# Optimization experiments

Hardware: AMD Instinct MI355X
Metric: run time of the kernel (lower is better)

Reference implementation:

```python
import jax, jax.numpy as jnp
import numpy as np

B, C, T, H, W = 8, 3, 16, 64, 64
CIN = C * T          # 48, conv in_channels
CQK = CIN // 8       # 6, query/key channels


def setup_inputs() -> dict:
    key = jax.random.key(0)
    ks = jax.random.split(key, 8)
    s = 0.05
    return {
        "x": jax.random.normal(ks[0], (B, C, T, H, W), dtype=jnp.float32),
        "Wq": jax.random.normal(ks[1], (CQK, CIN), dtype=jnp.float32) * s,
        "bq": jax.random.normal(ks[2], (CQK,), dtype=jnp.float32) * s,
        "Wk": jax.random.normal(ks[3], (CQK, CIN), dtype=jnp.float32) * s,
        "bk": jax.random.normal(ks[4], (CQK,), dtype=jnp.float32) * s,
        "Wv": jax.random.normal(ks[5], (CIN, CIN), dtype=jnp.float32) * s,
        "bv": jax.random.normal(ks[6], (CIN,), dtype=jnp.float32) * s,
        "gamma": jax.random.normal(ks[7], (1,), dtype=jnp.float32) * s,
    }


def reference(x, Wq, bq, Wk, bk, Wv, bv, gamma):
    b, c, t, h, w = x.shape
    n = h * w
    # merge channel and time dims: [B, C*T, H*W]
    x2 = x.reshape(b, c * t, n)
    # 1x1 convs are per-position channel matmuls
    q = jnp.einsum('oc,bcn->bon', Wq, x2) + bq[None, :, None]   # [B, CQK, N]
    k = jnp.einsum('oc,bcn->bon', Wk, x2) + bk[None, :, None]   # [B, CQK, N]
    v = jnp.einsum('oc,bcn->bon', Wv, x2) + bv[None, :, None]   # [B, CIN, N]
    # energy[b, i, j] = <q[:, i], k[:, j]>
    energy = jnp.einsum('bci,bcj->bij', q, k)                   # [B, N, N]
    attn = jax.nn.softmax(energy, axis=-1)
    # out[b, c, i] = sum_j v[b, c, j] * attn[b, i, j]
    out = jnp.einsum('bcj,bij->bci', v, attn)                   # [B, CIN, N]
    out = gamma[0] * out + x2
    return out.reshape(b, c, t, h, w)
```

## Files before the change

kernel.cpp:

```cpp
#include <hip/hip_runtime.h>

#define B_    8
#define CIN   48
#define CQK   6
#define N_    4096
#define CV    64
#define TI    64
#define TJ    64
#define NCH   4
#define JCH   (N_ / NCH)
#define TILES (JCH / TJ)

typedef __attribute__((ext_vector_type(8)))  short short8;
typedef __attribute__((ext_vector_type(16))) float f32x16;

__device__ __forceinline__ unsigned short f2bf(float f) {
    unsigned int u = __float_as_uint(f);
    u += 0x7FFFu + ((u >> 16) & 1u);
    return (unsigned short)(u >> 16);
}

__device__ __forceinline__ unsigned int cvt_pk_bf16(float a, float b) {
    unsigned int r;
    asm("v_cvt_pk_bf16_f32 %0, %1, %2" : "=v"(r) : "v"(a), "v"(b));
    return r;
}

__device__ __forceinline__ void pl32swap(unsigned int& x, unsigned int& y) {
    asm("v_permlane32_swap_b32 %0, %1" : "+v"(x), "+v"(y));
}

__device__ __forceinline__ short8 mk8(unsigned int w0, unsigned int w1,
                                      unsigned int w2, unsigned int w3) {
    union { unsigned int u[4]; short8 s; } t;
    t.u[0] = w0; t.u[1] = w1; t.u[2] = w2; t.u[3] = w3;
    return t.s;
}

__global__ __launch_bounds__(256) void qkv_kernel(
    const float* __restrict__ x,
    const float* __restrict__ Wq, const float* __restrict__ bq,
    const float* __restrict__ Wk, const float* __restrict__ bk,
    const float* __restrict__ Wv, const float* __restrict__ bv,
    unsigned short* __restrict__ qB, unsigned short* __restrict__ kB,
    unsigned short* __restrict__ vB)
{
    __shared__ float sWq[CQK * CIN], sWk[CQK * CIN], sWv[CIN * CIN];
    __shared__ float sbq[CQK], sbk[CQK], sbv[CIN];
    const int tid = threadIdx.x;
    for (int idx = tid; idx < CQK * CIN; idx += 256) { sWq[idx] = Wq[idx]; sWk[idx] = Wk[idx]; }
    for (int idx = tid; idx < CIN * CIN; idx += 256) sWv[idx] = Wv[idx];
    if (tid < CQK) { sbq[tid] = bq[tid]; sbk[tid] = bk[tid]; }
    if (tid < CIN) sbv[tid] = bv[tid];
    __syncthreads();

    const int b = blockIdx.x >> 6;
    const int g = tid >> 6;
    const int n = ((blockIdx.x & 63) << 6) + (tid & 63);

    float xc[CIN];
    const float* xb = x + ((size_t)b * CIN) * N_ + n;
#pragma unroll
    for (int c = 0; c < CIN; ++c) xc[c] = xb[(size_t)c * N_];

    if (g == 0) {
        short8 qrow = {0,0,0,0,0,0,0,0}, krow = {0,0,0,0,0,0,0,0};
#pragma unroll
        for (int o = 0; o < CQK; ++o) {
            float sq = sbq[o], sk = sbk[o];
#pragma unroll
            for (int c = 0; c < CIN; ++c) {
                sq += sWq[o * CIN + c] * xc[c];
                sk += sWk[o * CIN + c] * xc[c];
            }
            qrow[o] = (short)f2bf(sq);
            krow[o] = (short)f2bf(sk);
        }
        *(short8*)&qB[((size_t)b * N_ + n) * 8] = qrow;
        *(short8*)&kB[((size_t)b * N_ + n) * 8] = krow;
        vB[((size_t)b * CV + 48) * N_ + n] = 0x3F80u;
#pragma unroll
        for (int o = 49; o < CV; ++o) vB[((size_t)b * CV + o) * N_ + n] = 0;
    } else {
        const int o0 = (g - 1) * 16;
#pragma unroll
        for (int oo = 0; oo < 16; ++oo) {
            const int o = o0 + oo;
            float sv = sbv[o];
#pragma unroll
            for (int c = 0; c < CIN; ++c) sv += sWv[o * CIN + c] * xc[c];
            vB[((size_t)b * CV + o) * N_ + n] = f2bf(sv);
        }
    }
}

__global__ __launch_bounds__(512, 4) void attn_kernel(
    const unsigned short* __restrict__ qB, const unsigned short* __restrict__ kB,
    const unsigned short* __restrict__ vB, const float* __restrict__ x,
    const float* __restrict__ gamma, float* __restrict__ out)
{
    __shared__ unsigned short vt[NCH][CV][TJ];
    __shared__ float cbuf[CV][TI + 1];

    const int tid   = threadIdx.x;
    const int l     = tid & 63;
    const int w     = tid >> 6;
    const int chunk = w & 3;
    const int iw    = w >> 2;
    const int hi    = l >> 5;
    const int li    = l & 31;
    const int b     = blockIdx.x >> 6;
    const int ig    = blockIdx.x & 63;
    const int i_base = ig * TI;

    const unsigned short* kg = kB + (size_t)b * N_ * 8;
    const unsigned short* vg = vB + (size_t)b * CV * N_;

    short8 qf = {0,0,0,0,0,0,0,0};
    if (hi == 0)
        qf = *(const short8*)&qB[((size_t)b * N_ + i_base + iw * 32 + li) * 8];

    f32x16 zc, acc0, acc1;
#pragma unroll
    for (int r = 0; r < 16; ++r) { zc[r] = 0.f; acc0[r] = 0.f; acc1[r] = 0.f; }

#define DO_JST(JST, KF)                                                        \
    {                                                                          \
        f32x16 s = __builtin_amdgcn_mfma_f32_32x32x16_bf16(KF, qf, zc, 0, 0, 0);\
        _Pragma("unroll")                                                      \
        for (int r = 0; r < 16; ++r) s[r] = __expf(s[r]);                      \
        unsigned int c00 = cvt_pk_bf16(s[0],  s[1]);                           \
        unsigned int c10 = cvt_pk_bf16(s[2],  s[3]);                           \
        unsigned int c01 = cvt_pk_bf16(s[4],  s[5]);                           \
        unsigned int c11 = cvt_pk_bf16(s[6],  s[7]);                           \
        unsigned int c02 = cvt_pk_bf16(s[8],  s[9]);                           \
        unsigned int c12 = cvt_pk_bf16(s[10], s[11]);                          \
        unsigned int c03 = cvt_pk_bf16(s[12], s[13]);                          \
        unsigned int c13 = cvt_pk_bf16(s[14], s[15]);                          \
        unsigned int x0 = c00, y0 = c01; pl32swap(x0, y0);                     \
        unsigned int x1 = c10, y1 = c11; pl32swap(x1, y1);                     \
        const short8 pa0 = mk8(x0, x1, y0, y1);                                \
        unsigned int x2 = c02, y2 = c03; pl32swap(x2, y2);                     \
        unsigned int x3 = c12, y3 = c13; pl32swap(x3, y3);                     \
        const short8 pa1 = mk8(x2, x3, y2, y3);                                \
        const char* vrow0 = (const char*)&vt[chunk][li][0];                    \
        const char* vrow1 = (const char*)&vt[chunk][32 + li][0];               \
        short8 vf;                                                             \
        vf = *(const short8*)(vrow0 + ((((JST)*4 + 0 + hi) ^ (li & 7)) << 4)); \
        acc0 = __builtin_amdgcn_mfma_f32_32x32x16_bf16(pa0, vf, acc0, 0, 0, 0);\
        vf = *(const short8*)(vrow0 + ((((JST)*4 + 2 + hi) ^ (li & 7)) << 4)); \
        acc0 = __builtin_amdgcn_mfma_f32_32x32x16_bf16(pa1, vf, acc0, 0, 0, 0);\
        vf = *(const short8*)(vrow1 + ((((JST)*4 + 0 + hi) ^ (li & 7)) << 4)); \
        acc1 = __builtin_amdgcn_mfma_f32_32x32x16_bf16(pa0, vf, acc1, 0, 0, 0);\
        vf = *(const short8*)(vrow1 + ((((JST)*4 + 2 + hi) ^ (li & 7)) << 4)); \
        acc1 = __builtin_amdgcn_mfma_f32_32x32x16_bf16(pa1, vf, acc1, 0, 0, 0);\
    }

#pragma unroll 1
    for (int t = 0; t < TILES; ++t) {
        const int j0 = chunk * JCH + t * TJ;

        short8 kf0 = {0,0,0,0,0,0,0,0}, kf1 = {0,0,0,0,0,0,0,0};
        if (hi == 0) {
            kf0 = *(const short8*)&kg[(size_t)(j0 + li) * 8];
            kf1 = *(const short8*)&kg[(size_t)(j0 + 32 + li) * 8];
        }

        {
            const int tt = iw * 64 + l;
#pragma unroll
            for (int rep = 0; rep < 4; ++rep) {
                const int idx = tt + rep * 128;
                const int c   = idx >> 3;
                const int oc  = idx & 7;
                uint4 vdat = *(const uint4*)&vg[(size_t)c * N_ + j0 + oc * 8];
                *(uint4*)((char*)&vt[chunk][c][0] + ((oc ^ (c & 7)) << 4)) = vdat;
            }
        }
        __syncthreads();

        DO_JST(0, kf0)
        DO_JST(1, kf1)

        __syncthreads();
    }
#undef DO_JST

#pragma unroll 1
    for (int r = 0; r < NCH; ++r) {
        if (chunk == r) {
#pragma unroll
            for (int reg = 0; reg < 16; ++reg) {
                const int i_loc = iw * 32 + (reg & 3) + 8 * (reg >> 2) + 4 * hi;
                if (r == 0) {
                    cbuf[li][i_loc]      = acc0[reg];
                    cbuf[32 + li][i_loc] = acc1[reg];
                } else {
                    cbuf[li][i_loc]      += acc0[reg];
                    cbuf[32 + li][i_loc] += acc1[reg];
                }
            }
        }
        __syncthreads();
    }

    const float gm = gamma[0];
#pragma unroll
    for (int rep = 0; rep < 8; ++rep) {
        const int idx = tid + rep * 512;
        const int c   = idx >> 6;
        const int i2  = idx & 63;
        if (c < CIN) {
            const size_t off = ((size_t)b * CIN + c) * N_ + i_base + i2;
            out[off] = gm * (cbuf[c][i2] / cbuf[48][i2]) + x[off];
        }
    }
}

extern "C" void kernel_launch(void* const* d_in, const int* in_sizes, int n_in,
                              void* d_out, int out_size, void* d_ws, size_t ws_size,
                              hipStream_t stream)
{
    const float* x     = (const float*)d_in[0];
    const float* Wq    = (const float*)d_in[1];
    const float* bq    = (const float*)d_in[2];
    const float* Wk    = (const float*)d_in[3];
    const float* bk    = (const float*)d_in[4];
    const float* Wv    = (const float*)d_in[5];
    const float* bv    = (const float*)d_in[6];
    const float* gamma = (const float*)d_in[7];
    float* out = (float*)d_out;

    unsigned short* qB = (unsigned short*)d_ws;
    unsigned short* kB = qB + (size_t)B_ * N_ * 8;
    unsigned short* vB = kB + (size_t)B_ * N_ * 8;

    qkv_kernel<<<dim3(B_ * 64), dim3(256), 0, stream>>>(
        x, Wq, bq, Wk, bk, Wv, bv, qB, kB, vB);
    attn_kernel<<<dim3(B_ * 64), dim3(512), 0, stream>>>(
        qB, kB, vB, x, gamma, out);
}
```

Before: 56.29 us.

## Double-buffer V tiles via async global-to-LDS loads and split QKV projection work

The attention kernel now double-buffers the V tile in LDS, using global_load_lds direct copies issued one tile ahead, and prefetches the next K fragments into registers. This overlaps memory traffic with the MFMA/exp work and drops one barrier per tile. It also raises wave priority around the compute, reuses the V buffer for the reduction cbuf, and splits the QKV kernel across twice as many blocks to balance the per-thread projection work. The cost is doubled V LDS usage, which may affect occupancy, and extra x reloads in the QKV kernel.

```diff
diff --git a/kernel.cpp b/kernel.cpp
--- a/kernel.cpp
+++ b/kernel.cpp
@@ -35,6 +35,12 @@
     union { unsigned int u[4]; short8 s; } t;
     t.u[0] = w0; t.u[1] = w1; t.u[2] = w2; t.u[3] = w3;
     return t.s;
+}
+
+__device__ __forceinline__ void cp16(const unsigned short* g, unsigned short* l) {
+    __builtin_amdgcn_global_load_lds(
+        (const __attribute__((address_space(1))) unsigned int*)g,
+        (__attribute__((address_space(3))) unsigned int*)l, 16, 0, 0);
 }
 
 __global__ __launch_bounds__(256) void qkv_kernel(
@@ -54,37 +60,53 @@
     if (tid < CIN) sbv[tid] = bv[tid];
     __syncthreads();
 
-    const int b = blockIdx.x >> 6;
-    const int g = tid >> 6;
-    const int n = ((blockIdx.x & 63) << 6) + (tid & 63);
+    const int b   = blockIdx.x >> 7;
+    const int sub = blockIdx.x & 127;
+    const int pg  = sub >> 1;
+    const int p   = sub & 1;
+    const int g   = tid >> 6;
+    const int n   = (pg << 6) + (tid & 63);
 
     float xc[CIN];
     const float* xb = x + ((size_t)b * CIN) * N_ + n;
 #pragma unroll
     for (int c = 0; c < CIN; ++c) xc[c] = xb[(size_t)c * N_];
 
-    if (g == 0) {
-        short8 qrow = {0,0,0,0,0,0,0,0}, krow = {0,0,0,0,0,0,0,0};
-#pragma unroll
-        for (int o = 0; o < CQK; ++o) {
-            float sq = sbq[o], sk = sbk[o];
-#pragma unroll
-            for (int c = 0; c < CIN; ++c) {
-                sq += sWq[o * CIN + c] * xc[c];
-                sk += sWk[o * CIN + c] * xc[c];
-            }
-            qrow[o] = (short)f2bf(sq);
-            krow[o] = (short)f2bf(sk);
-        }
-        *(short8*)&qB[((size_t)b * N_ + n) * 8] = qrow;
-        *(short8*)&kB[((size_t)b * N_ + n) * 8] = krow;
-        vB[((size_t)b * CV + 48) * N_ + n] = 0x3F80u;
-#pragma unroll
-        for (int o = 49; o < CV; ++o) vB[((size_t)b * CV + o) * N_ + n] = 0;
+    if (p == 0) {
+        if (g < 2) {
+            const float* W  = g ? sWk : sWq;
+            const float* bb = g ? sbk : sbq;
+            short8 row = {0,0,0,0,0,0,0,0};
+#pragma unroll
+            for (int o = 0; o < CQK; ++o) {
+                float s = bb[o];
+#pragma unroll
+                for (int c = 0; c < CIN; ++c) s += W[o * CIN + c] * xc[c];
+                row[o] = (short)f2bf(s);
+            }
+            if (g == 0) {
+                *(short8*)&qB[((size_t)b * N_ + n) * 8] = row;
+                vB[((size_t)b * CV + 48) * N_ + n] = 0x3F80u;
+#pragma unroll
+                for (int o = 49; o < CV; ++o) vB[((size_t)b * CV + o) * N_ + n] = 0;
+            } else {
+                *(short8*)&kB[((size_t)b * N_ + n) * 8] = row;
+            }
+        } else {
+            const int o0 = (g - 2) * 8;
+#pragma unroll
+            for (int oo = 0; oo < 8; ++oo) {
+                const int o = o0 + oo;
+                float sv = sbv[o];
+#pragma unroll
+                for (int c = 0; c < CIN; ++c) sv += sWv[o * CIN + c] * xc[c];
+                vB[((size_t)b * CV + o) * N_ + n] = f2bf(sv);
+            }
+        }
     } else {
-        const int o0 = (g - 1) * 16;
-#pragma unroll
-        for (int oo = 0; oo < 16; ++oo) {
+        const int o0 = 16 + g * 8;
+#pragma unroll
+        for (int oo = 0; oo < 8; ++oo) {
             const int o = o0 + oo;
             float sv = sbv[o];
 #pragma unroll
@@ -99,8 +121,8 @@
     const unsigned short* __restrict__ vB, const float* __restrict__ x,
     const float* __restrict__ gamma, float* __restrict__ out)
 {
-    __shared__ unsigned short vt[NCH][CV][TJ];
-    __shared__ float cbuf[CV][TI + 1];
+    __shared__ __align__(16) unsigned short vt[2][NCH][CV][TJ];
+    float (*cbuf)[TI + 1] = (float (*)[TI + 1]) & vt[0][0][0][0];
 
     const int tid   = threadIdx.x;
     const int l     = tid & 63;
@@ -112,6 +134,7 @@
     const int b     = blockIdx.x >> 6;
     const int ig    = blockIdx.x & 63;
     const int i_base = ig * TI;
+    const int gx    = (l & 7) ^ ((l >> 3) & 7);
 
     const unsigned short* kg = kB + (size_t)b * N_ * 8;
     const unsigned short* vg = vB + (size_t)b * CV * N_;
@@ -124,7 +147,17 @@
 #pragma unroll
     for (int r = 0; r < 16; ++r) { zc[r] = 0.f; acc0[r] = 0.f; acc1[r] = 0.f; }
 
-#define DO_JST(JST, KF)                                                        \
+#define STAGE(BF, J0)                                                          \
+    {                                                                          \
+        _Pragma("unroll")                                                      \
+        for (int s = 0; s < 4; ++s) {                                          \
+            const int c = iw * 32 + s * 8 + (l >> 3);                          \
+            cp16(&vg[(size_t)c * N_ + (J0) + gx * 8],                          \
+                 &vt[BF][chunk][iw * 32 + s * 8][0]);                          \
+        }                                                                      \
+    }
+
+#define DO_JST(JST, KF, VTC)                                                   \
     {                                                                          \
         f32x16 s = __builtin_amdgcn_mfma_f32_32x32x16_bf16(KF, qf, zc, 0, 0, 0);\
         _Pragma("unroll")                                                      \
@@ -143,8 +176,8 @@
         unsigned int x2 = c02, y2 = c03; pl32swap(x2, y2);                     \
         unsigned int x3 = c12, y3 = c13; pl32swap(x3, y3);                     \
         const short8 pa1 = mk8(x2, x3, y2, y3);                                \
-        const char* vrow0 = (const char*)&vt[chunk][li][0];                    \
-        const char* vrow1 = (const char*)&vt[chunk][32 + li][0];               \
+        const char* vrow0 = (const char*)&(VTC)[li][0];                        \
+        const char* vrow1 = (const char*)&(VTC)[32 + li][0];                   \
         short8 vf;                                                             \
         vf = *(const short8*)(vrow0 + ((((JST)*4 + 0 + hi) ^ (li & 7)) << 4)); \
         acc0 = __builtin_amdgcn_mfma_f32_32x32x16_bf16(pa0, vf, acc0, 0, 0, 0);\
@@ -156,35 +189,38 @@
         acc1 = __builtin_amdgcn_mfma_f32_32x32x16_bf16(pa1, vf, acc1, 0, 0, 0);\
     }
 
+    const int jbase = chunk * JCH;
+    STAGE(0, jbase)
+    short8 kf0  = {0,0,0,0,0,0,0,0}, kf1  = {0,0,0,0,0,0,0,0};
+    short8 kf0n = {0,0,0,0,0,0,0,0}, kf1n = {0,0,0,0,0,0,0,0};
+    if (hi == 0) {
+        kf0 = *(const short8*)&kg[(size_t)(jbase + li) * 8];
+        kf1 = *(const short8*)&kg[(size_t)(jbase + 32 + li) * 8];
+    }
+    asm volatile("s_waitcnt vmcnt(0)" ::: "memory");
+    __syncthreads();
+
 #pragma unroll 1
     for (int t = 0; t < TILES; ++t) {
-        const int j0 = chunk * JCH + t * TJ;
-
-        short8 kf0 = {0,0,0,0,0,0,0,0}, kf1 = {0,0,0,0,0,0,0,0};
-        if (hi == 0) {
-            kf0 = *(const short8*)&kg[(size_t)(j0 + li) * 8];
-            kf1 = *(const short8*)&kg[(size_t)(j0 + 32 + li) * 8];
-        }
-
-        {
-            const int tt = iw * 64 + l;
-#pragma unroll
-            for (int rep = 0; rep < 4; ++rep) {
-                const int idx = tt + rep * 128;
-                const int c   = idx >> 3;
-                const int oc  = idx & 7;
-                uint4 vdat = *(const uint4*)&vg[(size_t)c * N_ + j0 + oc * 8];
-                *(uint4*)((char*)&vt[chunk][c][0] + ((oc ^ (c & 7)) << 4)) = vdat;
-            }
-        }
+        const int bf = t & 1;
+        if (t + 1 < TILES) {
+            const int j0n = jbase + (t + 1) * TJ;
+            STAGE(bf ^ 1, j0n)
+            if (hi == 0) {
+                kf0n = *(const short8*)&kg[(size_t)(j0n + li) * 8];
+                kf1n = *(const short8*)&kg[(size_t)(j0n + 32 + li) * 8];
+            }
+        }
+        __builtin_amdgcn_s_setprio(1);
+        DO_JST(0, kf0, vt[bf][chunk])
+        DO_JST(1, kf1, vt[bf][chunk])
+        __builtin_amdgcn_s_setprio(0);
+        asm volatile("s_waitcnt vmcnt(0)" ::: "memory");
         __syncthreads();
-
-        DO_JST(0, kf0)
-        DO_JST(1, kf1)
-
-        __syncthreads();
+        kf0 = kf0n; kf1 = kf1n;
     }
 #undef DO_JST
+#undef STAGE
 
 #pragma unroll 1
     for (int r = 0; r < NCH; ++r) {
@@ -235,7 +271,7 @@
     unsigned short* kB = qB + (size_t)B_ * N_ * 8;
     unsigned short* vB = kB + (size_t)B_ * N_ * 8;
 
-    qkv_kernel<<<dim3(B_ * 64), dim3(256), 0, stream>>>(
+    qkv_kernel<<<dim3(B_ * 128), dim3(256), 0, stream>>>(
         x, Wq, bq, Wk, bk, Wv, bv, qB, kB, vB);
     attn_kernel<<<dim3(B_ * 64), dim3(512), 0, stream>>>(
         qB, kB, vB, x, gamma, out);
```

New measurement: 56.53 us. About the same (+0.4%).
